# Optimization experiments

Measured on AMD Instinct MI355X. Metric: run time of the kernel, lower is better.

Reference implementation:

```python
import jax, jax.numpy as jnp
import numpy as np
import math

MEMORY_SIZE = 50000
FEATURE_SIZE = 4096  # = 64*8*8
HASH_SIZE = 128
B, C, H, W = 64, 64, 8, 8


def setup_inputs() -> dict:
    key = jax.random.key(0)
    k1, k2, k3, k4 = jax.random.split(key, 4)
    stdv = 1.0 / math.sqrt(FEATURE_SIZE)
    feature = jax.random.normal(k1, (B, C, H, W), dtype=jnp.float32)
    memory = jax.random.uniform(k2, (MEMORY_SIZE, FEATURE_SIZE), minval=-stdv, maxval=stdv, dtype=jnp.float32)
    # nn.Linear default init: U(-1/sqrt(fan_in), 1/sqrt(fan_in))
    hash_W = jax.random.uniform(k3, (HASH_SIZE, FEATURE_SIZE), minval=-stdv, maxval=stdv, dtype=jnp.float32)
    hash_b = jax.random.uniform(k4, (HASH_SIZE,), minval=-stdv, maxval=stdv, dtype=jnp.float32)
    return {"feature": feature, "memory": memory, "hash_W": hash_W, "hash_b": hash_b}


def _binarize(x, hash_W, hash_b):
    # 0.5 * (sign(Linear(x) - 0.5) + 1)  -> values in {0, 1} (0.5 only on measure-zero ties)
    return 0.5 * (jnp.sign(x @ hash_W.T + hash_b - 0.5) + 1.0)


def reference(feature, memory, hash_W, hash_b):
    b, c, h, w = feature.shape
    flat = feature.reshape(b, c * h * w)                      # [B, F]
    hm = _binarize(memory, hash_W, hash_b)                    # [M, 128]
    hf = _binarize(flat, hash_W, hash_b)                      # [B, 128]
    # For binary a,b: |a - b| = a + b - 2ab, so the L1 (Hamming) distance is a GEMM:
    HD = (hf.sum(-1, keepdims=True) + hm.sum(-1)[None, :]
          - 2.0 * (hf @ hm.T))                                # [B, M]
    idx = jnp.argmin(HD, axis=1)                              # [B]
    recon = memory[idx]                                       # gather nearest memory rows
    return recon.reshape(b, c, h, w)
```

## Files before the change

### kernel.cpp

```cpp
#include <hip/hip_runtime.h>
#include <hip/hip_bf16.h>
#include <stdint.h>
#include <stddef.h>

typedef __attribute__((ext_vector_type(8))) short s8v;
typedef __attribute__((ext_vector_type(4))) float f32x4;
typedef __attribute__((ext_vector_type(4))) uint32_t u32x4;
typedef __attribute__((ext_vector_type(4))) unsigned short u16x4;

#define KDIM 4096
#define NH   128
#define MMEM 50000
#define BFEAT 64
#define NGRP 3125
#define NBLK 256
#define NGMAX 13
#define NSEG 8

static __device__ __forceinline__ unsigned short f2bf(float f) {
  union { float f; uint32_t u; } c; c.f = f;
  uint32_t u = c.u;
  return (unsigned short)((u + 0x7FFFu + ((u >> 16) & 1u)) >> 16);
}

static __device__ __forceinline__ short f2bfs(float f) {
  __hip_bfloat16 h = __float2bfloat16(f);
  short s;
  __builtin_memcpy(&s, &h, sizeof(s));
  return s;
}

__global__ __launch_bounds__(256) void convert_w_kernel(
    const float* __restrict__ W, unsigned short* __restrict__ Wb,
    unsigned int* __restrict__ keys) {
  int i = blockIdx.x * 256 + threadIdx.x;
  if (blockIdx.x == 0 && threadIdx.x < BFEAT) keys[threadIdx.x] = 0xFFFFFFFFu;
  f32x4 v = reinterpret_cast<const f32x4*>(W)[i];
  u16x4 o;
  o[0] = f2bf(v[0]); o[1] = f2bf(v[1]); o[2] = f2bf(v[2]); o[3] = f2bf(v[3]);
  reinterpret_cast<u16x4*>(Wb)[i] = o;
}


__global__ __launch_bounds__(512, 2) void hash_bits_kernel(
    const float* __restrict__ A,
    const unsigned short* __restrict__ Wb,
    const float* __restrict__ hb,
    uint32_t* __restrict__ out_bits) {
  __shared__ short Abuf[2][NGMAX * 16 * 64];
  __shared__ unsigned short smb[NGMAX * 16][8];

  const int t    = threadIdx.x;
  const int lane = t & 63;
  const int w    = t >> 6;
  const int l15  = lane & 15;
  const int kq   = lane >> 4;
  const int b    = blockIdx.x;
  const int g0   = (b * NGRP) >> 8;
  const int NG   = (((b + 1) * NGRP) >> 8) - g0;
  const int row0 = g0 * 16;

  const float* srcA[4];
  int ldsoff[4];
#pragma unroll
  for (int p = 0; p < 4; ++p) {
    int P  = t + 512 * p;
    int g  = P >> 7;
    int q  = P & 127;
    int r  = q >> 3;
    int kg = q & 7;
    srcA[p]   = A + (size_t)(row0 + g * 16 + r) * KDIM + kg * 8;
    ldsoff[p] = (g * 16 + r) * 64 + ((kg ^ (r & 7)) << 3);
  }
  const bool v3 = (t + 1536) < NG * 128;

  const unsigned short* pb = Wb + (size_t)(16 * w + l15) * KDIM + kq * 8;
  const float hbv = hb[16 * w + l15];

  f32x4 acc[NGMAX];
#pragma unroll
  for (int g = 0; g < NGMAX; ++g) acc[g] = (f32x4){0.f, 0.f, 0.f, 0.f};

  f32x4 aR[4][2];
  s8v bA0, bA1, bB0, bB1;

#define LOADA(CH) do {                                                        \
  const f32x4* q0 = reinterpret_cast<const f32x4*>(srcA[0] + (CH) * 64);      \
  aR[0][0] = q0[0]; aR[0][1] = q0[1];                                         \
  const f32x4* q1 = reinterpret_cast<const f32x4*>(srcA[1] + (CH) * 64);      \
  aR[1][0] = q1[0]; aR[1][1] = q1[1];                                         \
  const f32x4* q2 = reinterpret_cast<const f32x4*>(srcA[2] + (CH) * 64);      \
  aR[2][0] = q2[0]; aR[2][1] = q2[1];                                         \
  if (v3) {                                                                   \
    const f32x4* q3 = reinterpret_cast<const f32x4*>(srcA[3] + (CH) * 64);    \
    aR[3][0] = q3[0]; aR[3][1] = q3[1];                                       \
  }                                                                           \
} while (0)

#define CVTW1(P, BUFW) do {                                                   \
  s8v av;                                                                     \
  av[0] = f2bfs(aR[P][0][0]); av[1] = f2bfs(aR[P][0][1]);                     \
  av[2] = f2bfs(aR[P][0][2]); av[3] = f2bfs(aR[P][0][3]);                     \
  av[4] = f2bfs(aR[P][1][0]); av[5] = f2bfs(aR[P][1][1]);                     \
  av[6] = f2bfs(aR[P][1][2]); av[7] = f2bfs(aR[P][1][3]);                     \
  *reinterpret_cast<s8v*>(&(BUFW)[ldsoff[P]]) = av;                           \
} while (0)

#define CVTWRITE(BUFW) do {                                                   \
  CVTW1(0, BUFW); CVTW1(1, BUFW); CVTW1(2, BUFW);                             \
  if (v3) CVTW1(3, BUFW);                                                     \
} while (0)

#define LOADB(CH, B0, B1) do {                                                \
  B0 = *reinterpret_cast<const s8v*>(pb + (CH) * 64);                         \
  B1 = *reinterpret_cast<const s8v*>(pb + (CH) * 64 + 32);                    \
} while (0)

#define COMPUTE(BUFR, B0, B1) do {                                            \
  _Pragma("unroll")                                                           \
  for (int g = 0; g < NGMAX; ++g) {                                           \
    const s8v af = *reinterpret_cast<const s8v*>(                             \
        &(BUFR)[(g * 16 + l15) * 64 + ((kq ^ (l15 & 7)) << 3)]);              \
    acc[g] = __builtin_amdgcn_mfma_f32_16x16x32_bf16(af, B0, acc[g], 0, 0, 0);\
  }                                                                           \
  _Pragma("unroll")                                                           \
  for (int g = 0; g < NGMAX; ++g) {                                           \
    const s8v af = *reinterpret_cast<const s8v*>(                             \
        &(BUFR)[(g * 16 + l15) * 64 + (((4 + kq) ^ (l15 & 7)) << 3)]);        \
    acc[g] = __builtin_amdgcn_mfma_f32_16x16x32_bf16(af, B1, acc[g], 0, 0, 0);\
  }                                                                           \
} while (0)

#define BARRIER() do {                                                        \
  asm volatile("s_waitcnt lgkmcnt(0)" ::: "memory");                          \
  __builtin_amdgcn_s_barrier();                                               \
  __builtin_amdgcn_sched_barrier(0);                                          \
} while (0)

#define STEP(S, BUFR, BUFW, B0, B1) do {                                      \
  BARRIER();                                                                  \
  COMPUTE(BUFR, B0, B1);                                                      \
  if ((S) + 1 < 64) CVTWRITE(BUFW);                                           \
  if ((S) + 2 < 64) { LOADA((S) + 2); LOADB((S) + 2, B0, B1); }               \
} while (0)

  LOADA(0);
  CVTWRITE(Abuf[0]);
  LOADA(1);
  LOADB(0, bA0, bA1);
  LOADB(1, bB0, bB1);

  for (int s2 = 0; s2 < 64; s2 += 2) {
    STEP(s2 + 0, Abuf[0], Abuf[1], bA0, bA1);
    STEP(s2 + 1, Abuf[1], Abuf[0], bB0, bB1);
  }

#pragma unroll
  for (int g = 0; g < NGMAX; ++g) {
#pragma unroll
    for (int r = 0; r < 4; ++r) {
      uint64_t mask = __ballot(acc[g][r] + hbv - 0.5f > 0.f);
      if (l15 == r)
        smb[g * 16 + (lane >> 4) * 4 + r][w] =
            (unsigned short)((mask >> (16 * (lane >> 4))) & 0xFFFFu);
    }
  }
  __syncthreads();
  const int rows = NG * 16;
  if (t < rows) {
    uint32_t w0 = (uint32_t)smb[t][0] | ((uint32_t)smb[t][1] << 16);
    uint32_t w1 = (uint32_t)smb[t][2] | ((uint32_t)smb[t][3] << 16);
    uint32_t w2 = (uint32_t)smb[t][4] | ((uint32_t)smb[t][5] << 16);
    uint32_t w3 = (uint32_t)smb[t][6] | ((uint32_t)smb[t][7] << 16);
    reinterpret_cast<u32x4*>(out_bits)[row0 + t] = (u32x4){w0, w1, w2, w3};
  }
}

__global__ __launch_bounds__(64) void hf_kernel(
    const float* __restrict__ flat, const float* __restrict__ W,
    const float* __restrict__ hb, unsigned char* __restrict__ hf_bytes) {
  int bid = blockIdx.x;
  int n = bid & 127, b = bid >> 7;
  int lane = threadIdx.x;
  const f32x4* fa = reinterpret_cast<const f32x4*>(flat + (size_t)b * KDIM);
  const f32x4* wa = reinterpret_cast<const f32x4*>(W + (size_t)n * KDIM);
  float s = 0.f;
#pragma unroll 4
  for (int q = 0; q < 16; ++q) {
    f32x4 x = fa[lane + 64 * q], y = wa[lane + 64 * q];
    s += x[0] * y[0] + x[1] * y[1] + x[2] * y[2] + x[3] * y[3];
  }
  for (int o = 32; o; o >>= 1) s += __shfl_down(s, o, 64);
  if (lane == 0) hf_bytes[b * NH + n] = (s + hb[n] - 0.5f) > 0.f ? 1 : 0;
}

__global__ __launch_bounds__(256) void argmin_part_kernel(
    const uint32_t* __restrict__ hm_bits, const unsigned char* __restrict__ hf_bytes,
    int M, unsigned int* __restrict__ keys) {
  __shared__ uint32_t red[256];
  const int b   = blockIdx.x & (BFEAT - 1);
  const int seg = blockIdx.x / BFEAT;
  const int span = (M + NSEG - 1) / NSEG;
  const int m0 = seg * span;
  int m1 = m0 + span; if (m1 > M) m1 = M;
  const int t = threadIdx.x;
  uint64_t hf0 = 0, hf1 = 0;
  const unsigned char* hfb = hf_bytes + b * NH;
  for (int c = 0; c < 64; ++c) {
    hf0 |= (uint64_t)(hfb[c] & 1u) << c;
    hf1 |= (uint64_t)(hfb[c + 64] & 1u) << c;
  }
  int hfsum = __popcll(hf0) + __popcll(hf1);
  uint32_t best = 0xFFFFFFFFu;
  for (int m = m0 + t; m < m1; m += 256) {
    u32x4 pv = reinterpret_cast<const u32x4*>(hm_bits)[m];
    uint64_t h0 = (uint64_t)pv[0] | ((uint64_t)pv[1] << 32);
    uint64_t h1 = (uint64_t)pv[2] | ((uint64_t)pv[3] << 32);
    int hmsum = __popcll(h0) + __popcll(h1);
    int dot   = __popcll(h0 & hf0) + __popcll(h1 & hf1);
    int hd    = hfsum + hmsum - 2 * dot;
    uint32_t key = ((uint32_t)hd << 16) | (uint32_t)m;
    best = best < key ? best : key;
  }
  red[t] = best;
  __syncthreads();
  for (int s = 128; s > 0; s >>= 1) {
    if (t < s) red[t] = red[t] < red[t + s] ? red[t] : red[t + s];
    __syncthreads();
  }
  if (t == 0) atomicMin(&keys[b], red[0]);
}

__global__ __launch_bounds__(256) void gather_kernel(
    const float* __restrict__ memory, const unsigned int* __restrict__ keys,
    float* __restrict__ out) {
  int b = blockIdx.x;
  int t = threadIdx.x;
  int m = (int)(keys[b] & 0xFFFFu);
  const f32x4* src = reinterpret_cast<const f32x4*>(memory + (size_t)m * KDIM);
  f32x4* dst = reinterpret_cast<f32x4*>(out + (size_t)b * KDIM);
#pragma unroll
  for (int c = 0; c < 4; ++c) dst[t + 256 * c] = src[t + 256 * c];
}

extern "C" void kernel_launch(void* const* d_in, const int* in_sizes, int n_in,
                              void* d_out, int out_size, void* d_ws, size_t ws_size,
                              hipStream_t stream) {
  const float* feature = (const float*)d_in[0];
  const float* memory  = (const float*)d_in[1];
  const float* hash_W  = (const float*)d_in[2];
  const float* hash_b  = (const float*)d_in[3];
  float* out = (float*)d_out;

  char* ws = (char*)d_ws;
  unsigned short* Wb       = (unsigned short*)ws;
  uint32_t*       hm_bits  = (uint32_t*)(ws + 1048576);
  unsigned char*  hf_bytes = (unsigned char*)(ws + 1048576 + 800000);
  unsigned int*   keys     = (unsigned int*)(ws + 1048576 + 800000 + 8192);

  convert_w_kernel<<<(NH * KDIM / 4) / 256, 256, 0, stream>>>(hash_W, Wb, keys);
  hash_bits_kernel<<<NBLK, 512, 0, stream>>>(memory, Wb, hash_b, hm_bits);
  hf_kernel<<<BFEAT * NH, 64, 0, stream>>>(feature, hash_W, hash_b, hf_bytes);
  argmin_part_kernel<<<BFEAT * NSEG, 256, 0, stream>>>(hm_bits, hf_bytes, MMEM, keys);
  gather_kernel<<<BFEAT, 256, 0, stream>>>(memory, keys, out);
}
```

Measured before the change: 191.0 us.

## Fuse hf projection into weight-convert kernel and deepen A-tile prefetch

```diff
diff --git a/kernel.cpp b/kernel.cpp
--- a/kernel.cpp
+++ b/kernel.cpp
@@ -30,15 +30,34 @@
   return s;
 }
 
-__global__ __launch_bounds__(256) void convert_w_kernel(
+__global__ __launch_bounds__(256) void prep_kernel(
     const float* __restrict__ W, unsigned short* __restrict__ Wb,
-    unsigned int* __restrict__ keys) {
-  int i = blockIdx.x * 256 + threadIdx.x;
-  if (blockIdx.x == 0 && threadIdx.x < BFEAT) keys[threadIdx.x] = 0xFFFFFFFFu;
-  f32x4 v = reinterpret_cast<const f32x4*>(W)[i];
-  u16x4 o;
-  o[0] = f2bf(v[0]); o[1] = f2bf(v[1]); o[2] = f2bf(v[2]); o[3] = f2bf(v[3]);
-  reinterpret_cast<u16x4*>(Wb)[i] = o;
+    const float* __restrict__ flat, const float* __restrict__ hb,
+    unsigned char* __restrict__ hf_bytes, unsigned int* __restrict__ keys) {
+  const int bid = blockIdx.x;
+  const int t   = threadIdx.x;
+  if (bid < 512) {
+    if (bid == 0 && t < BFEAT) keys[t] = 0xFFFFFFFFu;
+    int i = bid * 256 + t;
+    f32x4 v = reinterpret_cast<const f32x4*>(W)[i];
+    u16x4 o;
+    o[0] = f2bf(v[0]); o[1] = f2bf(v[1]); o[2] = f2bf(v[2]); o[3] = f2bf(v[3]);
+    reinterpret_cast<u16x4*>(Wb)[i] = o;
+  } else {
+    int did  = (bid - 512) * 4 + (t >> 6);
+    int n = did & 127, b = did >> 7;
+    int lane = t & 63;
+    const f32x4* fa = reinterpret_cast<const f32x4*>(flat + (size_t)b * KDIM);
+    const f32x4* wa = reinterpret_cast<const f32x4*>(W + (size_t)n * KDIM);
+    float s = 0.f;
+#pragma unroll 4
+    for (int q = 0; q < 16; ++q) {
+      f32x4 x = fa[lane + 64 * q], y = wa[lane + 64 * q];
+      s += x[0] * y[0] + x[1] * y[1] + x[2] * y[2] + x[3] * y[3];
+    }
+    for (int o = 32; o; o >>= 1) s += __shfl_down(s, o, 64);
+    if (lane == 0) hf_bytes[b * NH + n] = (s + hb[n] - 0.5f) > 0.f ? 1 : 0;
+  }
 }
 
 
@@ -81,34 +100,34 @@
 #pragma unroll
   for (int g = 0; g < NGMAX; ++g) acc[g] = (f32x4){0.f, 0.f, 0.f, 0.f};
 
-  f32x4 aR[4][2];
+  f32x4 aRA[4][2], aRB[4][2];
   s8v bA0, bA1, bB0, bB1;
 
-#define LOADA(CH) do {                                                        \
+#define LOADA_TO(SET, CH) do {                                                \
   const f32x4* q0 = reinterpret_cast<const f32x4*>(srcA[0] + (CH) * 64);      \
-  aR[0][0] = q0[0]; aR[0][1] = q0[1];                                         \
+  SET[0][0] = q0[0]; SET[0][1] = q0[1];                                       \
   const f32x4* q1 = reinterpret_cast<const f32x4*>(srcA[1] + (CH) * 64);      \
-  aR[1][0] = q1[0]; aR[1][1] = q1[1];                                         \
+  SET[1][0] = q1[0]; SET[1][1] = q1[1];                                       \
   const f32x4* q2 = reinterpret_cast<const f32x4*>(srcA[2] + (CH) * 64);      \
-  aR[2][0] = q2[0]; aR[2][1] = q2[1];                                         \
+  SET[2][0] = q2[0]; SET[2][1] = q2[1];                                       \
   if (v3) {                                                                   \
     const f32x4* q3 = reinterpret_cast<const f32x4*>(srcA[3] + (CH) * 64);    \
-    aR[3][0] = q3[0]; aR[3][1] = q3[1];                                       \
+    SET[3][0] = q3[0]; SET[3][1] = q3[1];                                     \
   }                                                                           \
 } while (0)
 
-#define CVTW1(P, BUFW) do {                                                   \
+#define CVTW1(SET, P, BUFW) do {                                              \
   s8v av;                                                                     \
-  av[0] = f2bfs(aR[P][0][0]); av[1] = f2bfs(aR[P][0][1]);                     \
-  av[2] = f2bfs(aR[P][0][2]); av[3] = f2bfs(aR[P][0][3]);                     \
-  av[4] = f2bfs(aR[P][1][0]); av[5] = f2bfs(aR[P][1][1]);                     \
-  av[6] = f2bfs(aR[P][1][2]); av[7] = f2bfs(aR[P][1][3]);                     \
+  av[0] = f2bfs(SET[P][0][0]); av[1] = f2bfs(SET[P][0][1]);                   \
+  av[2] = f2bfs(SET[P][0][2]); av[3] = f2bfs(SET[P][0][3]);                   \
+  av[4] = f2bfs(SET[P][1][0]); av[5] = f2bfs(SET[P][1][1]);                   \
+  av[6] = f2bfs(SET[P][1][2]); av[7] = f2bfs(SET[P][1][3]);                   \
   *reinterpret_cast<s8v*>(&(BUFW)[ldsoff[P]]) = av;                           \
 } while (0)
 
-#define CVTWRITE(BUFW) do {                                                   \
-  CVTW1(0, BUFW); CVTW1(1, BUFW); CVTW1(2, BUFW);                             \
-  if (v3) CVTW1(3, BUFW);                                                     \
+#define CVTWRITE(SET, BUFW) do {                                              \
+  CVTW1(SET, 0, BUFW); CVTW1(SET, 1, BUFW); CVTW1(SET, 2, BUFW);              \
+  if (v3) CVTW1(SET, 3, BUFW);                                                \
 } while (0)
 
 #define LOADB(CH, B0, B1) do {                                                \
@@ -137,22 +156,22 @@
   __builtin_amdgcn_sched_barrier(0);                                          \
 } while (0)
 
-#define STEP(S, BUFR, BUFW, B0, B1) do {                                      \
-  BARRIER();                                                                  \
-  COMPUTE(BUFR, B0, B1);                                                      \
-  if ((S) + 1 < 64) CVTWRITE(BUFW);                                           \
-  if ((S) + 2 < 64) { LOADA((S) + 2); LOADB((S) + 2, B0, B1); }               \
-} while (0)
-
-  LOADA(0);
-  CVTWRITE(Abuf[0]);
-  LOADA(1);
+  LOADA_TO(aRA, 0);
+  CVTWRITE(aRA, Abuf[0]);
+  LOADA_TO(aRB, 1);
   LOADB(0, bA0, bA1);
   LOADB(1, bB0, bB1);
 
   for (int s2 = 0; s2 < 64; s2 += 2) {
-    STEP(s2 + 0, Abuf[0], Abuf[1], bA0, bA1);
-    STEP(s2 + 1, Abuf[1], Abuf[0], bB0, bB1);
+    BARRIER();
+    COMPUTE(Abuf[0], bA0, bA1);
+    if (s2 + 1 < 64) CVTWRITE(aRB, Abuf[1]);
+    if (s2 + 3 < 64) { LOADA_TO(aRA, s2 + 2); LOADA_TO(aRB, s2 + 3); }
+    if (s2 + 2 < 64) LOADB(s2 + 2, bA0, bA1);
+    BARRIER();
+    COMPUTE(Abuf[1], bB0, bB1);
+    if (s2 + 2 < 64) CVTWRITE(aRA, Abuf[0]);
+    if (s2 + 3 < 64) LOADB(s2 + 3, bB0, bB1);
   }
 
 #pragma unroll
@@ -174,24 +193,6 @@
     uint32_t w3 = (uint32_t)smb[t][6] | ((uint32_t)smb[t][7] << 16);
     reinterpret_cast<u32x4*>(out_bits)[row0 + t] = (u32x4){w0, w1, w2, w3};
   }
-}
-
-__global__ __launch_bounds__(64) void hf_kernel(
-    const float* __restrict__ flat, const float* __restrict__ W,
-    const float* __restrict__ hb, unsigned char* __restrict__ hf_bytes) {
-  int bid = blockIdx.x;
-  int n = bid & 127, b = bid >> 7;
-  int lane = threadIdx.x;
-  const f32x4* fa = reinterpret_cast<const f32x4*>(flat + (size_t)b * KDIM);
-  const f32x4* wa = reinterpret_cast<const f32x4*>(W + (size_t)n * KDIM);
-  float s = 0.f;
-#pragma unroll 4
-  for (int q = 0; q < 16; ++q) {
-    f32x4 x = fa[lane + 64 * q], y = wa[lane + 64 * q];
-    s += x[0] * y[0] + x[1] * y[1] + x[2] * y[2] + x[3] * y[3];
-  }
-  for (int o = 32; o; o >>= 1) s += __shfl_down(s, o, 64);
-  if (lane == 0) hf_bytes[b * NH + n] = (s + hb[n] - 0.5f) > 0.f ? 1 : 0;
 }
 
 __global__ __launch_bounds__(256) void argmin_part_kernel(
@@ -258,9 +259,8 @@
   unsigned char*  hf_bytes = (unsigned char*)(ws + 1048576 + 800000);
   unsigned int*   keys     = (unsigned int*)(ws + 1048576 + 800000 + 8192);
 
-  convert_w_kernel<<<(NH * KDIM / 4) / 256, 256, 0, stream>>>(hash_W, Wb, keys);
+  prep_kernel<<<2560, 256, 0, stream>>>(hash_W, Wb, feature, hash_b, hf_bytes, keys);
   hash_bits_kernel<<<NBLK, 512, 0, stream>>>(memory, Wb, hash_b, hm_bits);
-  hf_kernel<<<BFEAT * NH, 64, 0, stream>>>(feature, hash_W, hash_b, hf_bytes);
   argmin_part_kernel<<<BFEAT * NSEG, 256, 0, stream>>>(hm_bits, hf_bytes, MMEM, keys);
   gather_kernel<<<BFEAT, 256, 0, stream>>>(memory, keys, out);
 }
```

After: 204.3 us. 1.07x slower.

## Fuse hf projection into prep kernel and stagger K-chunk order per block

Applied to the files above, without the earlier changes.

```diff
diff --git a/kernel.cpp b/kernel.cpp
--- a/kernel.cpp
+++ b/kernel.cpp
@@ -30,15 +30,34 @@
   return s;
 }
 
-__global__ __launch_bounds__(256) void convert_w_kernel(
+__global__ __launch_bounds__(256) void prep_kernel(
     const float* __restrict__ W, unsigned short* __restrict__ Wb,
-    unsigned int* __restrict__ keys) {
-  int i = blockIdx.x * 256 + threadIdx.x;
-  if (blockIdx.x == 0 && threadIdx.x < BFEAT) keys[threadIdx.x] = 0xFFFFFFFFu;
-  f32x4 v = reinterpret_cast<const f32x4*>(W)[i];
-  u16x4 o;
-  o[0] = f2bf(v[0]); o[1] = f2bf(v[1]); o[2] = f2bf(v[2]); o[3] = f2bf(v[3]);
-  reinterpret_cast<u16x4*>(Wb)[i] = o;
+    const float* __restrict__ flat, const float* __restrict__ hb,
+    unsigned char* __restrict__ hf_bytes, unsigned int* __restrict__ keys) {
+  const int bid = blockIdx.x;
+  const int t   = threadIdx.x;
+  if (bid < 512) {
+    if (bid == 0 && t < BFEAT) keys[t] = 0xFFFFFFFFu;
+    int i = bid * 256 + t;
+    f32x4 v = reinterpret_cast<const f32x4*>(W)[i];
+    u16x4 o;
+    o[0] = f2bf(v[0]); o[1] = f2bf(v[1]); o[2] = f2bf(v[2]); o[3] = f2bf(v[3]);
+    reinterpret_cast<u16x4*>(Wb)[i] = o;
+  } else {
+    int did  = (bid - 512) * 4 + (t >> 6);
+    int n = did & 127, b = did >> 7;
+    int lane = t & 63;
+    const f32x4* fa = reinterpret_cast<const f32x4*>(flat + (size_t)b * KDIM);
+    const f32x4* wa = reinterpret_cast<const f32x4*>(W + (size_t)n * KDIM);
+    float s = 0.f;
+#pragma unroll 4
+    for (int q = 0; q < 16; ++q) {
+      f32x4 x = fa[lane + 64 * q], y = wa[lane + 64 * q];
+      s += x[0] * y[0] + x[1] * y[1] + x[2] * y[2] + x[3] * y[3];
+    }
+    for (int o = 32; o; o >>= 1) s += __shfl_down(s, o, 64);
+    if (lane == 0) hf_bytes[b * NH + n] = (s + hb[n] - 0.5f) > 0.f ? 1 : 0;
+  }
 }
 
 
@@ -56,6 +75,7 @@
   const int l15  = lane & 15;
   const int kq   = lane >> 4;
   const int b    = blockIdx.x;
+  const int koff = b & 63;
   const int g0   = (b * NGRP) >> 8;
   const int NG   = (((b + 1) * NGRP) >> 8) - g0;
   const int row0 = g0 * 16;
@@ -83,6 +103,8 @@
 
   f32x4 aR[4][2];
   s8v bA0, bA1, bB0, bB1;
+
+#define PCH(S) (((S) + koff) & 63)
 
 #define LOADA(CH) do {                                                        \
   const f32x4* q0 = reinterpret_cast<const f32x4*>(srcA[0] + (CH) * 64);      \
@@ -141,14 +163,14 @@
   BARRIER();                                                                  \
   COMPUTE(BUFR, B0, B1);                                                      \
   if ((S) + 1 < 64) CVTWRITE(BUFW);                                           \
-  if ((S) + 2 < 64) { LOADA((S) + 2); LOADB((S) + 2, B0, B1); }               \
-} while (0)
-
-  LOADA(0);
+  if ((S) + 2 < 64) { LOADA(PCH((S) + 2)); LOADB(PCH((S) + 2), B0, B1); }     \
+} while (0)
+
+  LOADA(PCH(0));
   CVTWRITE(Abuf[0]);
-  LOADA(1);
-  LOADB(0, bA0, bA1);
-  LOADB(1, bB0, bB1);
+  LOADA(PCH(1));
+  LOADB(PCH(0), bA0, bA1);
+  LOADB(PCH(1), bB0, bB1);
 
   for (int s2 = 0; s2 < 64; s2 += 2) {
     STEP(s2 + 0, Abuf[0], Abuf[1], bA0, bA1);
@@ -174,24 +196,6 @@
     uint32_t w3 = (uint32_t)smb[t][6] | ((uint32_t)smb[t][7] << 16);
     reinterpret_cast<u32x4*>(out_bits)[row0 + t] = (u32x4){w0, w1, w2, w3};
   }
-}
-
-__global__ __launch_bounds__(64) void hf_kernel(
-    const float* __restrict__ flat, const float* __restrict__ W,
-    const float* __restrict__ hb, unsigned char* __restrict__ hf_bytes) {
-  int bid = blockIdx.x;
-  int n = bid & 127, b = bid >> 7;
-  int lane = threadIdx.x;
-  const f32x4* fa = reinterpret_cast<const f32x4*>(flat + (size_t)b * KDIM);
-  const f32x4* wa = reinterpret_cast<const f32x4*>(W + (size_t)n * KDIM);
-  float s = 0.f;
-#pragma unroll 4
-  for (int q = 0; q < 16; ++q) {
-    f32x4 x = fa[lane + 64 * q], y = wa[lane + 64 * q];
-    s += x[0] * y[0] + x[1] * y[1] + x[2] * y[2] + x[3] * y[3];
-  }
-  for (int o = 32; o; o >>= 1) s += __shfl_down(s, o, 64);
-  if (lane == 0) hf_bytes[b * NH + n] = (s + hb[n] - 0.5f) > 0.f ? 1 : 0;
 }
 
 __global__ __launch_bounds__(256) void argmin_part_kernel(
@@ -258,9 +262,8 @@
   unsigned char*  hf_bytes = (unsigned char*)(ws + 1048576 + 800000);
   unsigned int*   keys     = (unsigned int*)(ws + 1048576 + 800000 + 8192);
 
-  convert_w_kernel<<<(NH * KDIM / 4) / 256, 256, 0, stream>>>(hash_W, Wb, keys);
+  prep_kernel<<<2560, 256, 0, stream>>>(hash_W, Wb, feature, hash_b, hf_bytes, keys);
   hash_bits_kernel<<<NBLK, 512, 0, stream>>>(memory, Wb, hash_b, hm_bits);
-  hf_kernel<<<BFEAT * NH, 64, 0, stream>>>(feature, hash_W, hash_b, hf_bytes);
   argmin_part_kernel<<<BFEAT * NSEG, 256, 0, stream>>>(hm_bits, hf_bytes, MMEM, keys);
   gather_kernel<<<BFEAT, 256, 0, stream>>>(memory, keys, out);
 }
```

Result: faster. 175.2 us, median of 2 (-8.3%).
